# Performance work log

Measured on AMD Instinct MI355X. Metric: run time of the kernel, lower is better.

## Reference

```python
import jax, jax.numpy as jnp
import numpy as np

B, L, G, D = 32, 128, 64, 256
HD = 128; H = 2 * HD          # bidirectional LSTM hidden
N, K = 8, 4                   # nodes per graph, idx per node
NINP, NHID, NREL = 128, 32, 16
NTOK = 1000
E = B * N * N                 # all-pairs edges per graph, flattened
EPS = 1e-5


def setup_inputs() -> dict:
    key = jax.random.key(0)
    ks = jax.random.split(key, 40)
    rn = lambda i, shape, s: (s * jax.random.normal(ks[i], shape)).astype(jnp.float32)
    inp = {}
    inp["seq"] = jax.random.randint(ks[0], (B, L), 0, NTOK, dtype=jnp.int32)
    inp["pos2grp"] = jax.random.randint(ks[1], (B, L), 0, G, dtype=jnp.int32)
    inp["idx"] = jax.random.randint(ks[2], (B, N, K), 0, L, dtype=jnp.int32)
    ii = np.repeat(np.arange(N), N); jj = np.tile(np.arange(N), N)
    inp["u"] = jnp.asarray((np.arange(B)[:, None] * N + ii[None, :]).reshape(-1), dtype=jnp.int32)
    inp["v"] = jnp.asarray((np.arange(B)[:, None] * N + jj[None, :]).reshape(-1), dtype=jnp.int32)
    inp["mask"] = jax.random.uniform(ks[3], (E, NREL)) < 0.1
    inp["emb"] = rn(4, (NTOK, D), 1.0)
    # BiLSTM params (1 layer, 2 directions); gate order i,f,g,o
    inp["Wih_f"] = rn(5, (4 * HD, D), 0.05); inp["Whh_f"] = rn(6, (4 * HD, HD), 0.05)
    inp["bih_f"] = jnp.zeros((4 * HD,), jnp.float32); inp["bhh_f"] = jnp.zeros((4 * HD,), jnp.float32)
    inp["Wih_b"] = rn(7, (4 * HD, D), 0.05); inp["Whh_b"] = rn(8, (4 * HD, HD), 0.05)
    inp["bih_b"] = jnp.zeros((4 * HD,), jnp.float32); inp["bhh_b"] = jnp.zeros((4 * HD,), jnp.float32)
    inp["lin_src_w"] = rn(9, (NINP, H), 0.05); inp["lin_src_b"] = jnp.zeros((NINP,), jnp.float32)
    inp["lin_dst_w"] = rn(10, (NINP, H), 0.05); inp["lin_dst_b"] = jnp.zeros((NINP,), jnp.float32)
    inp["bn_src_g"] = jnp.ones((NINP,), jnp.float32); inp["bn_src_b"] = jnp.zeros((NINP,), jnp.float32)
    inp["bn_dst_g"] = jnp.ones((NINP,), jnp.float32); inp["bn_dst_b"] = jnp.zeros((NINP,), jnp.float32)
    inp["ntl_w"] = rn(11, (NREL, NHID, NINP, NINP), 0.001)
    inp["ntl_v"] = rn(12, (NREL, NHID, 2 * NINP), 0.001)
    inp["ntl_b"] = jnp.zeros((NREL, NHID, 1), jnp.float32)
    inp["ntl_u"] = rn(13, (NREL, 1, NHID), 0.001)
    inp["ntl_bn_g"] = jnp.ones((NREL * NHID,), jnp.float32)
    inp["ntl_bn_b"] = jnp.zeros((NREL * NHID,), jnp.float32)
    return inp


def _lstm(xs, Wih, Whh, bih, bhh):
    # xs: (T, B, D) -> (T, B, HD)
    nb = xs.shape[1]
    def step(carry, xt):
        h, c = carry
        g = xt @ Wih.T + h @ Whh.T + bih + bhh
        i, f, gg, o = jnp.split(g, 4, axis=-1)
        c = jax.nn.sigmoid(f) * c + jax.nn.sigmoid(i) * jnp.tanh(gg)
        h = jax.nn.sigmoid(o) * jnp.tanh(c)
        return (h, c), h
    init = (jnp.zeros((nb, HD), xs.dtype), jnp.zeros((nb, HD), xs.dtype))
    _, hs = jax.lax.scan(step, init, xs)
    return hs


def _bn(x, g, b):
    # training-mode BatchNorm1d over axis 0 (biased variance, as torch)
    m = x.mean(0)
    v = x.var(0)
    return (x - m) * jax.lax.rsqrt(v + EPS) * g + b


def _forward(emb, Wih_f, Whh_f, bih_f, bhh_f, Wih_b, Whh_b, bih_b, bhh_b,
             lin_src_w, lin_src_b, lin_dst_w, lin_dst_b,
             bn_src_g, bn_src_b, bn_dst_g, bn_dst_b,
             ntl_w, ntl_v, ntl_b, ntl_u, ntl_bn_g, ntl_bn_b,
             seq, pos2grp, idx, u, v):
    # 1) token embedding + scatter_sum into groups
    x_tok = emb[seq]                                         # (B,L,D)
    flat_ids = (pos2grp + jnp.arange(B, dtype=pos2grp.dtype)[:, None] * G).reshape(-1)
    x_grp = jax.ops.segment_sum(x_tok.reshape(B * L, D), flat_ids,
                                num_segments=B * G).reshape(B, G, D)
    # 2) BiLSTM over group sequence
    xs = x_grp.transpose(1, 0, 2)                            # (G,B,D)
    hf = _lstm(xs, Wih_f, Whh_f, bih_f, bhh_f)
    hb = _lstm(xs[::-1], Wih_b, Whh_b, bih_b, bhh_b)[::-1]
    h_grp = jnp.concatenate([hf, hb], -1).transpose(1, 0, 2) # (B,G,H)
    # 3) fancy-indexed gather h_grp[i, pos2grp[i, idx], :] + scatter_sum over K
    grp_of_idx = jnp.take_along_axis(pos2grp, idx.reshape(B, N * K), axis=1)
    h_sel = jnp.take_along_axis(h_grp, grp_of_idx[..., None], axis=1)  # (B,N*K,H)
    h = h_sel.reshape(B, N, K, H).sum(2).reshape(B * N, H)
    # 4) per-endpoint projection + batchnorm
    hd = _bn(h[u] @ lin_src_w.T + lin_src_b, bn_src_g, bn_src_b)  # (E,NINP)
    tl = _bn(h[v] @ lin_dst_w.T + lin_dst_b, bn_dst_g, bn_dst_b)
    # 5) neural tensor layer (bilinear=True)
    cat = jnp.concatenate([hd, tl], 1)                       # (E,2*NINP)
    linear = jnp.einsum('rhi,ei->rhe', ntl_v, cat)
    tmp = jnp.einsum('rhij,ei->rhej', ntl_w, hd)             # (NREL,NHID,E,NINP)
    bilinear = jnp.einsum('rhej,ej->rhe', tmp, tl)
    pre = bilinear + linear + ntl_b                          # (NREL,NHID,E)
    flat = pre.reshape(NREL * NHID, E).T                     # (E, NREL*NHID)
    act = jnp.tanh(_bn(flat, ntl_bn_g, ntl_bn_b).T.reshape(NREL, NHID, E))
    logit = jnp.einsum('rh,rhe->er', ntl_u[:, 0, :], act)    # (E,NREL)
    return logit


def reference(seq, pos2grp, idx, u, v, mask, emb,
              Wih_f, Whh_f, bih_f, bhh_f, Wih_b, Whh_b, bih_b, bhh_b,
              lin_src_w, lin_src_b, lin_dst_w, lin_dst_b,
              bn_src_g, bn_src_b, bn_dst_g, bn_dst_b,
              ntl_w, ntl_v, ntl_b, ntl_u, ntl_bn_g, ntl_bn_b):
    logit = _forward(emb, Wih_f, Whh_f, bih_f, bhh_f, Wih_b, Whh_b, bih_b, bhh_b,
                     lin_src_w, lin_src_b, lin_dst_w, lin_dst_b,
                     bn_src_g, bn_src_b, bn_dst_g, bn_dst_b,
                     ntl_w, ntl_v, ntl_b, ntl_u, ntl_bn_g, ntl_bn_b,
                     seq, pos2grp, idx, u, v)
    gt = logit > 0
    eq = gt == mask
    acc = eq.astype(jnp.float32).mean()
    gid = jnp.repeat(jnp.arange(B, dtype=jnp.int32), N * N)
    em = jax.ops.segment_min(jnp.all(eq, 1).astype(jnp.int32), gid, num_segments=B)
    emr = em.astype(jnp.float32).mean()
    nll_pos = -jnp.sum(jnp.where(mask, jax.nn.log_sigmoid(logit), 0.0)) / B
    nll_neg = -jnp.sum(jnp.where(mask, 0.0, jnp.log(1.0 + 1e-5 - jax.nn.sigmoid(logit)))) / B
    loss = nll_pos + nll_neg
    return logit, loss, acc, emr
```

## Files before the change

### kernel.cpp

```cpp
#include <hip/hip_runtime.h>
#include <math.h>

namespace {

constexpr int cB = 32, cL = 128, cG = 64, cD = 256;
constexpr int cHD = 128, cH = 256;
constexpr int cN = 8, cK = 4;
constexpr int cNI = 128, cRH = 512;
constexpr int cE = 2048;
constexpr float cEPS = 1e-5f;

typedef __bf16 bf16x8 __attribute__((ext_vector_type(8)));
typedef float f32x4 __attribute__((ext_vector_type(4)));

__device__ __forceinline__ f32x4 mfma16(bf16x8 a, bf16x8 b, f32x4 c) {
    return __builtin_amdgcn_mfma_f32_16x16x32_bf16(a, b, c, 0, 0, 0);
}

__device__ __forceinline__ float bf2f(unsigned short u) {
    unsigned int x = ((unsigned int)u) << 16;
    return __uint_as_float(x);
}
__device__ __forceinline__ unsigned short f2bf(float f) {
    unsigned int x = __float_as_uint(f);
    unsigned int r = (x + 0x7fffu + ((x >> 16) & 1u)) >> 16;
    return (unsigned short)r;
}
__device__ __forceinline__ float frcp(float x) { return __builtin_amdgcn_rcpf(x); }
__device__ __forceinline__ float fsig(float x) { return frcp(1.f + __expf(-x)); }
__device__ __forceinline__ float ftanh(float x) { return 1.f - 2.f * frcp(__expf(2.f * x) + 1.f); }
__device__ __forceinline__ float nls(float x) {
    return (x >= 0.f) ? log1pf(expf(-x)) : (log1pf(expf(x)) - x);
}
__device__ __forceinline__ bf16x8 cvt8(const float* __restrict__ p) {
    float4 a = *(const float4*)p, b = *(const float4*)(p + 4);
    bf16x8 v;
    v[0] = (__bf16)a.x; v[1] = (__bf16)a.y; v[2] = (__bf16)a.z; v[3] = (__bf16)a.w;
    v[4] = (__bf16)b.x; v[5] = (__bf16)b.y; v[6] = (__bf16)b.z; v[7] = (__bf16)b.w;
    return v;
}

__device__ __forceinline__ void bar_lgkm() {
    asm volatile("s_waitcnt lgkmcnt(0)\n\ts_barrier" ::: "memory");
}

__global__ void k_embed(const int* __restrict__ seq, const int* __restrict__ p2g,
                        const float* __restrict__ emb, float* __restrict__ x_seq) {
    __shared__ float xl[cG * cD];
    int b = blockIdx.x, t = threadIdx.x;
    for (int g = 0; g < cG; ++g) xl[g * cD + t] = 0.f;
    for (int l = 0; l < cL; ++l) {
        int tok = seq[b * cL + l];
        int g = p2g[b * cL + l];
        xl[g * cD + t] += emb[tok * cD + t];
    }
    for (int g = 0; g < cG; ++g)
        x_seq[(g * cB + b) * cD + t] = xl[g * cD + t];
}

__global__ __launch_bounds__(512) void k_gemm_in(
    const float* __restrict__ x_seq,
    const float* __restrict__ wih_f, const float* __restrict__ wih_b,
    const float* __restrict__ bih_f, const float* __restrict__ bhh_f,
    const float* __restrict__ bih_b, const float* __restrict__ bhh_b,
    float* __restrict__ pre) {
    int ns = blockIdx.x, g = blockIdx.y;
    int t = threadIdx.x;
    int w = t >> 6, l = t & 63, lc = l & 15, lk = l >> 4;
    int gn = ns * 128 + w * 16 + lc;
    const float* wrow = (gn < 512) ? (wih_f + (size_t)gn * cD)
                                   : (wih_b + (size_t)(gn - 512) * cD);
    const float* xb0 = x_seq + ((size_t)g * 32 + lc) * cD;
    const float* xb1 = x_seq + ((size_t)g * 32 + 16 + lc) * cD;
    f32x4 acc0 = {0.f, 0.f, 0.f, 0.f}, acc1 = {0.f, 0.f, 0.f, 0.f};
#pragma unroll
    for (int kf = 0; kf < 8; ++kf) {
        int ko = kf * 32 + lk * 8;
        bf16x8 a = cvt8(wrow + ko);
        bf16x8 b0 = cvt8(xb0 + ko);
        bf16x8 b1 = cvt8(xb1 + ko);
        acc0 = mfma16(a, b0, acc0);
        acc1 = mfma16(a, b1, acc1);
    }
    int nb = ns * 128 + w * 16 + lk * 4;
    float4 bv;
    if (nb < 512) {
        float4 u = *(const float4*)(bih_f + nb);
        float4 v = *(const float4*)(bhh_f + nb);
        bv = make_float4(u.x + v.x, u.y + v.y, u.z + v.z, u.w + v.w);
    } else {
        float4 u = *(const float4*)(bih_b + nb - 512);
        float4 v = *(const float4*)(bhh_b + nb - 512);
        bv = make_float4(u.x + v.x, u.y + v.y, u.z + v.z, u.w + v.w);
    }
    size_t base = ((size_t)g * 256 + (nb >> 2)) * 32;
    *(float4*)(pre + (base + lc) * 4) =
        make_float4(acc0[0] + bv.x, acc0[1] + bv.y, acc0[2] + bv.z, acc0[3] + bv.w);
    *(float4*)(pre + (base + 16 + lc) * 4) =
        make_float4(acc1[0] + bv.x, acc1[1] + bv.y, acc1[2] + bv.z, acc1[3] + bv.w);
}

__device__ __forceinline__ void lstm_step(
    f32x4 (&acc)[4], float (&cst)[4], const bf16x8 (&wf)[4][4],
    const unsigned short* __restrict__ hr, unsigned short* __restrict__ hw,
    const int (&rdo)[4], int wro,
    const float* __restrict__ preb, int gpre, bool dopre,
    unsigned short* __restrict__ hob, int g) {
    bf16x8 hf[4];
#pragma unroll
    for (int kf = 0; kf < 4; ++kf)
        hf[kf] = *(const bf16x8*)((const char*)hr + rdo[kf]);
#pragma unroll
    for (int kf = 0; kf < 4; ++kf)
#pragma unroll
        for (int q = 0; q < 4; ++q)
            acc[q] = mfma16(wf[q][kf], hf[kf], acc[q]);
    float hv[4];
#pragma unroll
    for (int r = 0; r < 4; ++r) {
        float ig = fsig(acc[0][r]);
        float fg = fsig(acc[1][r]);
        float gg = ftanh(acc[2][r]);
        float og = fsig(acc[3][r]);
        float cv = fg * cst[r] + ig * gg;
        cst[r] = cv;
        hv[r] = og * ftanh(cv);
    }
    if (dopre) {
#pragma unroll
        for (int q = 0; q < 4; ++q)
            acc[q] = *(const f32x4*)(preb + (size_t)gpre * 32768 + q * 4096);
    }
    unsigned int p0 = (unsigned int)f2bf(hv[0]) | ((unsigned int)f2bf(hv[1]) << 16);
    unsigned int p1 = (unsigned int)f2bf(hv[2]) | ((unsigned int)f2bf(hv[3]) << 16);
    *(uint2*)((char*)hw + wro) = make_uint2(p0, p1);
    *(uint2*)(hob + (size_t)g * 8192) = make_uint2(p0, p1);
    bar_lgkm();
}

__global__ __launch_bounds__(512, 2) void k_lstm_m(
    const float* __restrict__ pre,
    const float* __restrict__ whh_f, const float* __restrict__ whh_b,
    unsigned short* __restrict__ h_out) {
    __shared__ __align__(16) unsigned short hl[2][2048];
    int t = threadIdx.x;
    int w = t >> 6, l = t & 63, lc = l & 15, lk = l >> 4;
    int dir = blockIdx.x >> 1, bg = (blockIdx.x & 1) * 16;
    const float* whh = dir ? whh_b : whh_f;
    bf16x8 wf[4][4];
#pragma unroll
    for (int q = 0; q < 4; ++q) {
        int n = q * 128 + w * 16 + lc;
#pragma unroll
        for (int kf = 0; kf < 4; ++kf)
            wf[q][kf] = cvt8(whh + (size_t)n * 128 + kf * 32 + lk * 8);
    }
    *(uint2*)&hl[1][t * 4] = make_uint2(0u, 0u);
    const float* preb = pre + ((size_t)(dir * 128 + w * 4 + lk) * 32 + (bg + lc)) * 4;
    unsigned short* hob = h_out + ((size_t)(dir * 32 + bg + lc) * 128 + w * 16 + lk * 4);
    int rdo[4];
#pragma unroll
    for (int kf = 0; kf < 4; ++kf)
        rdo[kf] = (lc * 256 + kf * 64 + lk * 16) ^ (lc << 4);
    int wro = (lc * 256 + w * 32 + lk * 8) ^ (lc << 4);
    f32x4 accA[4], accB[4];
    float cst[4] = {0.f, 0.f, 0.f, 0.f};
    int g0 = dir ? 63 : 0;
    int sgn = dir ? -1 : 1;
#pragma unroll
    for (int q = 0; q < 4; ++q) accA[q] = *(const f32x4*)(preb + (size_t)g0 * 32768 + q * 4096);
#pragma unroll
    for (int q = 0; q < 4; ++q) accB[q] = *(const f32x4*)(preb + (size_t)(g0 + sgn) * 32768 + q * 4096);
    bar_lgkm();
    for (int s = 0; s < 64; s += 2) {
        int ga = g0 + sgn * s;
        lstm_step(accA, cst, wf, hl[1], hl[0], rdo, wro, preb, ga + 2 * sgn, s < 62, hob, ga);
        lstm_step(accB, cst, wf, hl[0], hl[1], rdo, wro, preb, ga + 3 * sgn, s < 61, hob, ga + sgn);
    }
}

__global__ __launch_bounds__(256) void k_gather(
    const int* __restrict__ idx, const int* __restrict__ p2g,
    const unsigned short* __restrict__ h_out, float* __restrict__ hsumT) {
    __shared__ float xr[32][257];
    int n0 = blockIdx.x * 32, t = threadIdx.x;
    int dirq = t >> 7, hh = t & 127;
    for (int nl = 0; nl < 32; ++nl) {
        int bn = n0 + nl;
        int b = bn >> 3;
        float acc = 0.f;
#pragma unroll
        for (int k = 0; k < cK; ++k) {
            int l = idx[bn * cK + k];
            int g = p2g[b * cL + l];
            acc += bf2f(h_out[(size_t)g * 8192 + (size_t)(dirq * 32 + b) * 128 + hh]);
        }
        xr[nl][t] = acc;
    }
    __syncthreads();
    int c_hi = t >> 5, nl = t & 31;
    for (int rep = 0; rep < 32; ++rep) {
        int c = rep * 8 + c_hi;
        hsumT[(size_t)c * 256 + n0 + nl] = xr[nl][c];
    }
}

__global__ __launch_bounds__(256) void k_proj_bn(
    const float* __restrict__ hsumT,
    const float* __restrict__ w_src, const float* __restrict__ b_src,
    const float* __restrict__ w_dst, const float* __restrict__ b_dst,
    const float* __restrict__ g_src, const float* __restrict__ bb_src,
    const float* __restrict__ g_dst, const float* __restrict__ bb_dst,
    float* __restrict__ hd_bn, float* __restrict__ tl_bn) {
    int which = blockIdx.x, c = blockIdx.y, t = threadIdx.x;
    __shared__ float ws[256];
    __shared__ float ssum[256], ssq[256];
    ws[t] = (which ? w_dst : w_src)[(size_t)c * cH + t];
    __syncthreads();
    float acc = (which ? b_dst : b_src)[c];
#pragma unroll 8
    for (int k = 0; k < cH; ++k)
        acc += ws[k] * hsumT[(size_t)k * 256 + t];
    ssum[t] = acc;
    ssq[t] = acc * acc;
    __syncthreads();
    for (int o = 128; o > 0; o >>= 1) {
        if (t < o) { ssum[t] += ssum[t + o]; ssq[t] += ssq[t + o]; }
        __syncthreads();
    }
    float mean = ssum[0] * (1.f / 256.f);
    float var = ssq[0] * (1.f / 256.f) - mean * mean;
    float gam = which ? g_dst[c] : g_src[c];
    float bet = which ? bb_dst[c] : bb_src[c];
    float scale = gam * rsqrtf(var + cEPS);
    (which ? tl_bn : hd_bn)[(size_t)t * cNI + c] = (acc - mean) * scale + bet;
}

__global__ __launch_bounds__(256, 2) void k_ntl_A(
    const float* __restrict__ hd_bn, const float* __restrict__ tl_bn,
    const float* __restrict__ ntl_w, const float* __restrict__ ntl_v,
    unsigned short* __restrict__ tmp,
    float* __restrict__ lsrc, float* __restrict__ ldst) {
    __shared__ __align__(16) unsigned short wl[128 * 128];
    __shared__ float vsh[256];
    int rh = blockIdx.x, t = threadIdx.x;
    int w = t >> 6, l = t & 63, lc = l & 15, lk = l >> 4;
    vsh[t] = ntl_v[(size_t)rh * 256 + t];
    {
        const float* wbase = ntl_w + (size_t)rh * 16384;
        int k = t >> 1, c0 = (t & 1) * 64;
        int sw = ((k >> 3) & 3) << 4;
#pragma unroll
        for (int u = 0; u < 8; ++u) {
            bf16x8 v = cvt8(wbase + k * 128 + c0 + u * 8);
            *(bf16x8*)((char*)wl + ((k * 256 + (c0 + u * 8) * 2) ^ sw)) = v;
        }
    }
    __syncthreads();
    {
        const float* hr = hd_bn + (size_t)t * cNI;
        const float* tr = tl_bn + (size_t)t * cNI;
        float a1 = 0.f, a2 = 0.f;
#pragma unroll 8
        for (int i = 0; i < cNI; i += 4) {
            float4 h4 = *(const float4*)(hr + i);
            float4 t4 = *(const float4*)(tr + i);
            a1 += h4.x * vsh[i] + h4.y * vsh[i + 1] + h4.z * vsh[i + 2] + h4.w * vsh[i + 3];
            a2 += t4.x * vsh[128 + i] + t4.y * vsh[128 + i + 1] + t4.z * vsh[128 + i + 2] + t4.w * vsh[128 + i + 3];
        }
        lsrc[(size_t)rh * 256 + t] = a1;
        ldst[(size_t)rh * 256 + t] = a2;
    }
    f32x4 acc[4][8] = {};
#pragma unroll
    for (int kf = 0; kf < 4; ++kf) {
        bf16x8 af[4];
#pragma unroll
        for (int mt = 0; mt < 4; ++mt) {
            int m = w * 64 + mt * 16 + lc;
            af[mt] = cvt8(hd_bn + (size_t)m * 128 + kf * 32 + lk * 8);
        }
#pragma unroll
        for (int nt = 0; nt < 8; ++nt) {
            int kb = (kf * 32 + lk * 8) * 256;
            int jb = (nt * 16 + lc) * 2;
            bf16x8 bv = *(const bf16x8*)((char*)wl + ((kb + jb) ^ (lk << 4)));
#pragma unroll
            for (int mt = 0; mt < 4; ++mt) acc[mt][nt] = mfma16(af[mt], bv, acc[mt][nt]);
        }
    }
#pragma unroll
    for (int mt = 0; mt < 4; ++mt) {
#pragma unroll
        for (int nt = 0; nt < 8; ++nt) {
            unsigned int lo = (unsigned int)f2bf(acc[mt][nt][0]) | ((unsigned int)f2bf(acc[mt][nt][1]) << 16);
            unsigned int hi = (unsigned int)f2bf(acc[mt][nt][2]) | ((unsigned int)f2bf(acc[mt][nt][3]) << 16);
            size_t off = (size_t)rh * 32768 + (size_t)((((w * 4 + mt) * 8 + nt) * 64 + l) * 4);
            *(uint2*)(tmp + off) = make_uint2(lo, hi);
        }
    }
}

__global__ __launch_bounds__(256) void k_ntl_B(
    const unsigned short* __restrict__ tmp, const float* __restrict__ tl_bn,
    const float* __restrict__ lsrc, const float* __restrict__ ldst,
    const float* __restrict__ ntl_b, float* __restrict__ pre2) {
    int bgid = blockIdx.x;
    int rh = blockIdx.y;
    int t = threadIdx.x;
    int n0 = bgid * 32;
    __shared__ float tm[32][132];
    __shared__ float tl[32][132];
    {
        const uint4* src = (const uint4*)(tmp + (size_t)rh * 32768 +
                                          (size_t)(bgid >> 1) * 8192 + (size_t)(bgid & 1) * 4096);
#pragma unroll
        for (int rep = 0; rep < 2; ++rep) {
            int q = t + rep * 256;
            uint4 uv = src[q];
            unsigned int wds[4] = {uv.x, uv.y, uv.z, uv.w};
            int e0 = q * 8;
#pragma unroll
            for (int ui = 0; ui < 4; ++ui) {
                int e = e0 + ui * 2;
                int mt_l = e >> 11;
                int nt = (e >> 8) & 7;
                int ln = (e >> 2) & 63;
                int r = e & 3;
                int m = mt_l * 16 + (ln >> 4) * 4 + r;
                int j = nt * 16 + (ln & 15);
                tm[m][j] = bf2f((unsigned short)(wds[ui] & 0xffff));
                tm[m + 1][j] = bf2f((unsigned short)(wds[ui] >> 16));
            }
        }
        int r = t >> 3;
        int c0 = (t & 7) * 16;
        const float4* fsrc = (const float4*)(tl_bn + (size_t)(n0 + r) * cNI + c0);
        float4 f0 = fsrc[0], f1 = fsrc[1], f2v = fsrc[2], f3 = fsrc[3];
        float* frow = &tl[r][c0];
        frow[0] = f0.x; frow[1] = f0.y; frow[2] = f0.z; frow[3] = f0.w;
        frow[4] = f1.x; frow[5] = f1.y; frow[6] = f1.z; frow[7] = f1.w;
        frow[8] = f2v.x; frow[9] = f2v.y; frow[10] = f2v.z; frow[11] = f2v.w;
        frow[12] = f3.x; frow[13] = f3.y; frow[14] = f3.z; frow[15] = f3.w;
    }
    __syncthreads();
    int b_l = t >> 6, p = t & 63, i = p >> 3, j = p & 7;
    const float* ta = &tm[b_l * 8 + i][0];
    const float* tb = &tl[b_l * 8 + j][0];
    float s = 0.f;
#pragma unroll 8
    for (int k = 0; k < 128; ++k) s += ta[k] * tb[k];
    int e = bgid * 256 + t;
    int bglob = bgid * 4 + b_l;
    int un = bglob * 8 + i, vn = bglob * 8 + j;
    pre2[(size_t)rh * cE + e] = s + lsrc[(size_t)rh * 256 + un] + ldst[(size_t)rh * 256 + vn] + ntl_b[rh];
}

__global__ void k_bn2(const float* __restrict__ pre2,
                      const float* __restrict__ g, const float* __restrict__ bta,
                      float* __restrict__ scale, float* __restrict__ shift) {
    int rh = blockIdx.x, t = threadIdx.x;
    const float* row = pre2 + (size_t)rh * cE;
    float s = 0.f, q = 0.f;
#pragma unroll
    for (int ii = 0; ii < 8; ++ii) {
        float v = row[ii * 256 + t];
        s += v; q += v * v;
    }
    __shared__ float ssum[256], ssq[256];
    ssum[t] = s; ssq[t] = q;
    __syncthreads();
    for (int o = 128; o > 0; o >>= 1) {
        if (t < o) { ssum[t] += ssum[t + o]; ssq[t] += ssq[t + o]; }
        __syncthreads();
    }
    if (t == 0) {
        float mean = ssum[0] * (1.f / 2048.f);
        float var = ssq[0] * (1.f / 2048.f) - mean * mean;
        float sc = g[rh] * rsqrtf(var + cEPS);
        scale[rh] = sc;
        shift[rh] = bta[rh] - mean * sc;
    }
}

__global__ __launch_bounds__(256) void k_final(
    const float* __restrict__ pre2,
    const float* __restrict__ scale, const float* __restrict__ shift,
    const float* __restrict__ ntl_u, const int* __restrict__ mask,
    float* __restrict__ out, float* __restrict__ part) {
    int r = blockIdx.y, et = blockIdx.x;
    int t = threadIdx.x;
    int e = et * 256 + t;
    float a = 0.f;
#pragma unroll
    for (int h = 0; h < 32; ++h) {
        int rh = r * 32 + h;
        float p = pre2[(size_t)rh * cE + e];
        a += ntl_u[rh] * ftanh(fmaf(p, scale[rh], shift[rh]));
    }
    out[(size_t)e * 16 + r] = a;
    int m = mask[(size_t)e * 16 + r];
    bool mb = (m != 0);
    bool eq = ((a > 0.f) == mb);
    float nll = mb ? nls(a) : -logf(1.f / (1.f + expf(a)) + 1e-5f);
    float corr = eq ? 1.f : 0.f;
    unsigned long long bal = __ballot(eq);
    float em = (bal == ~0ull) ? 1.f : 0.f;
#pragma unroll
    for (int o = 32; o > 0; o >>= 1) {
        nll += __shfl_down(nll, o);
        corr += __shfl_down(corr, o);
    }
    if ((t & 63) == 0) {
        int bg = et * 4 + (t >> 6);
        float* p = part + ((size_t)bg * 16 + r) * 4;
        p[0] = nll; p[1] = corr; p[2] = em;
    }
}

__global__ void k_loss_fin(const float* __restrict__ part, float* __restrict__ out) {
    int t = threadIdx.x;
    float nll = 0.f, corr = 0.f, em = 0.f;
    if (t < 32) {
        em = 1.f;
        for (int r = 0; r < 16; ++r) {
            const float* p = part + ((size_t)t * 16 + r) * 4;
            nll += p[0]; corr += p[1]; em = fminf(em, p[2]);
        }
    }
#pragma unroll
    for (int o = 32; o > 0; o >>= 1) {
        nll += __shfl_down(nll, o);
        corr += __shfl_down(corr, o);
        em += __shfl_down(em, o);
    }
    if (t == 0) {
        out[32768] = nll / 32.f;
        out[32769] = corr / 32768.f;
        out[32770] = em / 32.f;
    }
}

}

extern "C" void kernel_launch(void* const* d_in, const int* in_sizes, int n_in,
                              void* d_out, int out_size, void* d_ws, size_t ws_size,
                              hipStream_t stream) {
    (void)in_sizes; (void)n_in; (void)out_size; (void)ws_size;
    const int* seq = (const int*)d_in[0];
    const int* p2g = (const int*)d_in[1];
    const int* idx = (const int*)d_in[2];
    const int* mask = (const int*)d_in[5];
    const float* emb = (const float*)d_in[6];
    const float* wih_f = (const float*)d_in[7];
    const float* whh_f = (const float*)d_in[8];
    const float* bih_f = (const float*)d_in[9];
    const float* bhh_f = (const float*)d_in[10];
    const float* wih_b = (const float*)d_in[11];
    const float* whh_b = (const float*)d_in[12];
    const float* bih_b = (const float*)d_in[13];
    const float* bhh_b = (const float*)d_in[14];
    const float* lsw = (const float*)d_in[15];
    const float* lsb = (const float*)d_in[16];
    const float* ldw = (const float*)d_in[17];
    const float* ldb = (const float*)d_in[18];
    const float* bn_sg = (const float*)d_in[19];
    const float* bn_sb = (const float*)d_in[20];
    const float* bn_dg = (const float*)d_in[21];
    const float* bn_db = (const float*)d_in[22];
    const float* ntlw = (const float*)d_in[23];
    const float* ntlv = (const float*)d_in[24];
    const float* ntlb = (const float*)d_in[25];
    const float* ntlu = (const float*)d_in[26];
    const float* bn2g = (const float*)d_in[27];
    const float* bn2b = (const float*)d_in[28];
    float* out = (float*)d_out;
    char* ws = (char*)d_ws;

    float* x_seq = (float*)(ws + 0);
    float* pre = (float*)(ws + 2097152);
    unsigned short* tmp = (unsigned short*)(ws + 0);
    size_t off = 33554432;
    unsigned short* h_out = (unsigned short*)(ws + off); off += 1048576;
    float* hsumT = (float*)(ws + off); off += 262144;
    float* hd_bn = (float*)(ws + off); off += 131072;
    float* tl_bn = (float*)(ws + off); off += 131072;
    float* lsrc = (float*)(ws + off); off += 524288;
    float* ldst = (float*)(ws + off); off += 524288;
    float* pre2 = (float*)(ws + off); off += 4194304;
    float* scale = (float*)(ws + off); off += 2048;
    float* shift = (float*)(ws + off); off += 2048;
    float* part = (float*)(ws + off); off += 8192;

    k_embed<<<32, 256, 0, stream>>>(seq, p2g, emb, x_seq);
    k_gemm_in<<<dim3(8, 64), 512, 0, stream>>>(x_seq, wih_f, wih_b, bih_f, bhh_f, bih_b, bhh_b, pre);
    k_lstm_m<<<4, 512, 0, stream>>>(pre, whh_f, whh_b, h_out);
    k_gather<<<8, 256, 0, stream>>>(idx, p2g, h_out, hsumT);
    k_proj_bn<<<dim3(2, 128), 256, 0, stream>>>(hsumT, lsw, lsb, ldw, ldb,
                                                bn_sg, bn_sb, bn_dg, bn_db, hd_bn, tl_bn);
    k_ntl_A<<<512, 256, 0, stream>>>(hd_bn, tl_bn, ntlw, ntlv, tmp, lsrc, ldst);
    k_ntl_B<<<dim3(8, 512), 256, 0, stream>>>(tmp, tl_bn, lsrc, ldst, ntlb, pre2);
    k_bn2<<<512, 256, 0, stream>>>(pre2, bn2g, bn2b, scale, shift);
    k_final<<<dim3(8, 16), 256, 0, stream>>>(pre2, scale, shift, ntlu, mask, out, part);
    k_loss_fin<<<1, 64, 0, stream>>>(part, out);
}
```

Baseline: 190.7 us.

## Fuse BN2 stats into ntl_B, parallelize gather, batch embed loads

Removes the separate k_bn2 kernel. k_ntl_B now uses 64-thread blocks that each compute a 2x2 register tile of outputs and write per-block partial sum and sum-of-squares. k_final reduces those partials into BN scale and shift in shared memory. k_gather now launches one block per node instead of 8 blocks that loop over 32 nodes, and k_embed stages token and group indices in shared memory and issues four embedding loads per iteration. These changes aim to cut one launch plus a full read of pre2 and to raise parallelism in the small kernels, at the cost of uncoalesced transposed stores in gather and fewer threads per block in ntl_B.

New measurement: 178.1 us. 6.6% less time.

```diff
diff --git a/kernel.cpp b/kernel.cpp
--- a/kernel.cpp
+++ b/kernel.cpp
@@ -44,15 +44,25 @@
     asm volatile("s_waitcnt lgkmcnt(0)\n\ts_barrier" ::: "memory");
 }
 
-__global__ void k_embed(const int* __restrict__ seq, const int* __restrict__ p2g,
-                        const float* __restrict__ emb, float* __restrict__ x_seq) {
+__global__ __launch_bounds__(256) void k_embed(
+    const int* __restrict__ seq, const int* __restrict__ p2g,
+    const float* __restrict__ emb, float* __restrict__ x_seq) {
     __shared__ float xl[cG * cD];
+    __shared__ int toks[cL], grps[cL];
     int b = blockIdx.x, t = threadIdx.x;
+    if (t < 128) toks[t] = seq[b * cL + t];
+    else grps[t - 128] = p2g[b * cL + (t - 128)];
     for (int g = 0; g < cG; ++g) xl[g * cD + t] = 0.f;
-    for (int l = 0; l < cL; ++l) {
-        int tok = seq[b * cL + l];
-        int g = p2g[b * cL + l];
-        xl[g * cD + t] += emb[tok * cD + t];
+    __syncthreads();
+    for (int l = 0; l < cL; l += 4) {
+        float v0 = emb[(size_t)toks[l + 0] * cD + t];
+        float v1 = emb[(size_t)toks[l + 1] * cD + t];
+        float v2 = emb[(size_t)toks[l + 2] * cD + t];
+        float v3 = emb[(size_t)toks[l + 3] * cD + t];
+        xl[grps[l + 0] * cD + t] += v0;
+        xl[grps[l + 1] * cD + t] += v1;
+        xl[grps[l + 2] * cD + t] += v2;
+        xl[grps[l + 3] * cD + t] += v3;
     }
     for (int g = 0; g < cG; ++g)
         x_seq[(g * cB + b) * cD + t] = xl[g * cD + t];
@@ -182,27 +192,18 @@
 __global__ __launch_bounds__(256) void k_gather(
     const int* __restrict__ idx, const int* __restrict__ p2g,
     const unsigned short* __restrict__ h_out, float* __restrict__ hsumT) {
-    __shared__ float xr[32][257];
-    int n0 = blockIdx.x * 32, t = threadIdx.x;
+    int bn = blockIdx.x;
+    int b = bn >> 3;
+    int t = threadIdx.x;
     int dirq = t >> 7, hh = t & 127;
-    for (int nl = 0; nl < 32; ++nl) {
-        int bn = n0 + nl;
-        int b = bn >> 3;
-        float acc = 0.f;
-#pragma unroll
-        for (int k = 0; k < cK; ++k) {
-            int l = idx[bn * cK + k];
-            int g = p2g[b * cL + l];
-            acc += bf2f(h_out[(size_t)g * 8192 + (size_t)(dirq * 32 + b) * 128 + hh]);
-        }
-        xr[nl][t] = acc;
-    }
-    __syncthreads();
-    int c_hi = t >> 5, nl = t & 31;
-    for (int rep = 0; rep < 32; ++rep) {
-        int c = rep * 8 + c_hi;
-        hsumT[(size_t)c * 256 + n0 + nl] = xr[nl][c];
-    }
+    int l0 = idx[bn * cK + 0], l1 = idx[bn * cK + 1];
+    int l2 = idx[bn * cK + 2], l3 = idx[bn * cK + 3];
+    int g0 = p2g[b * cL + l0], g1 = p2g[b * cL + l1];
+    int g2 = p2g[b * cL + l2], g3 = p2g[b * cL + l3];
+    size_t ro = (size_t)(dirq * 32 + b) * 128 + hh;
+    float a = bf2f(h_out[(size_t)g0 * 8192 + ro]) + bf2f(h_out[(size_t)g1 * 8192 + ro]) +
+              bf2f(h_out[(size_t)g2 * 8192 + ro]) + bf2f(h_out[(size_t)g3 * 8192 + ro]);
+    hsumT[(size_t)t * 256 + bn] = a;
 }
 
 __global__ __launch_bounds__(256) void k_proj_bn(
@@ -301,10 +302,11 @@
     }
 }
 
-__global__ __launch_bounds__(256) void k_ntl_B(
+__global__ __launch_bounds__(64) void k_ntl_B(
     const unsigned short* __restrict__ tmp, const float* __restrict__ tl_bn,
     const float* __restrict__ lsrc, const float* __restrict__ ldst,
-    const float* __restrict__ ntl_b, float* __restrict__ pre2) {
+    const float* __restrict__ ntl_b, float* __restrict__ pre2,
+    float2* __restrict__ part2) {
     int bgid = blockIdx.x;
     int rh = blockIdx.y;
     int t = threadIdx.x;
@@ -315,8 +317,8 @@
         const uint4* src = (const uint4*)(tmp + (size_t)rh * 32768 +
                                           (size_t)(bgid >> 1) * 8192 + (size_t)(bgid & 1) * 4096);
 #pragma unroll
-        for (int rep = 0; rep < 2; ++rep) {
-            int q = t + rep * 256;
+        for (int rep = 0; rep < 8; ++rep) {
+            int q = t + rep * 64;
             uint4 uv = src[q];
             unsigned int wds[4] = {uv.x, uv.y, uv.z, uv.w};
             int e0 = q * 8;
@@ -333,70 +335,88 @@
                 tm[m + 1][j] = bf2f((unsigned short)(wds[ui] >> 16));
             }
         }
-        int r = t >> 3;
-        int c0 = (t & 7) * 16;
-        const float4* fsrc = (const float4*)(tl_bn + (size_t)(n0 + r) * cNI + c0);
-        float4 f0 = fsrc[0], f1 = fsrc[1], f2v = fsrc[2], f3 = fsrc[3];
-        float* frow = &tl[r][c0];
-        frow[0] = f0.x; frow[1] = f0.y; frow[2] = f0.z; frow[3] = f0.w;
-        frow[4] = f1.x; frow[5] = f1.y; frow[6] = f1.z; frow[7] = f1.w;
-        frow[8] = f2v.x; frow[9] = f2v.y; frow[10] = f2v.z; frow[11] = f2v.w;
-        frow[12] = f3.x; frow[13] = f3.y; frow[14] = f3.z; frow[15] = f3.w;
+#pragma unroll
+        for (int rep = 0; rep < 4; ++rep) {
+            int tt = t + rep * 64;
+            int r = tt >> 3;
+            int c0 = (tt & 7) * 16;
+            const float4* fsrc = (const float4*)(tl_bn + (size_t)(n0 + r) * cNI + c0);
+            float4 f0 = fsrc[0], f1 = fsrc[1], f2v = fsrc[2], f3 = fsrc[3];
+            float* frow = &tl[r][c0];
+            frow[0] = f0.x; frow[1] = f0.y; frow[2] = f0.z; frow[3] = f0.w;
+            frow[4] = f1.x; frow[5] = f1.y; frow[6] = f1.z; frow[7] = f1.w;
+            frow[8] = f2v.x; frow[9] = f2v.y; frow[10] = f2v.z; frow[11] = f2v.w;
+            frow[12] = f3.x; frow[13] = f3.y; frow[14] = f3.z; frow[15] = f3.w;
+        }
     }
     __syncthreads();
-    int b_l = t >> 6, p = t & 63, i = p >> 3, j = p & 7;
-    const float* ta = &tm[b_l * 8 + i][0];
-    const float* tb = &tl[b_l * 8 + j][0];
-    float s = 0.f;
-#pragma unroll 8
-    for (int k = 0; k < 128; ++k) s += ta[k] * tb[k];
-    int e = bgid * 256 + t;
+    int b_l = t >> 4, i2 = (t >> 2) & 3, j2 = t & 3;
+    const float* ta0 = &tm[b_l * 8 + i2][0];
+    const float* ta1 = &tm[b_l * 8 + i2 + 4][0];
+    const float* tb0 = &tl[b_l * 8 + j2][0];
+    const float* tb1 = &tl[b_l * 8 + j2 + 4][0];
+    float s00 = 0.f, s01 = 0.f, s10 = 0.f, s11 = 0.f;
+#pragma unroll 4
+    for (int k = 0; k < 128; ++k) {
+        float a0 = ta0[k], a1 = ta1[k], b0 = tb0[k], b1 = tb1[k];
+        s00 += a0 * b0; s01 += a0 * b1; s10 += a1 * b0; s11 += a1 * b1;
+    }
     int bglob = bgid * 4 + b_l;
-    int un = bglob * 8 + i, vn = bglob * 8 + j;
-    pre2[(size_t)rh * cE + e] = s + lsrc[(size_t)rh * 256 + un] + ldst[(size_t)rh * 256 + vn] + ntl_b[rh];
-}
-
-__global__ void k_bn2(const float* __restrict__ pre2,
-                      const float* __restrict__ g, const float* __restrict__ bta,
-                      float* __restrict__ scale, float* __restrict__ shift) {
-    int rh = blockIdx.x, t = threadIdx.x;
-    const float* row = pre2 + (size_t)rh * cE;
-    float s = 0.f, q = 0.f;
-#pragma unroll
-    for (int ii = 0; ii < 8; ++ii) {
-        float v = row[ii * 256 + t];
-        s += v; q += v * v;
-    }
-    __shared__ float ssum[256], ssq[256];
-    ssum[t] = s; ssq[t] = q;
-    __syncthreads();
-    for (int o = 128; o > 0; o >>= 1) {
-        if (t < o) { ssum[t] += ssum[t + o]; ssq[t] += ssq[t + o]; }
-        __syncthreads();
-    }
-    if (t == 0) {
-        float mean = ssum[0] * (1.f / 2048.f);
-        float var = ssq[0] * (1.f / 2048.f) - mean * mean;
-        float sc = g[rh] * rsqrtf(var + cEPS);
-        scale[rh] = sc;
-        shift[rh] = bta[rh] - mean * sc;
-    }
+    float nb = ntl_b[rh];
+    const float* ls = lsrc + (size_t)rh * 256 + bglob * 8;
+    const float* ld = ldst + (size_t)rh * 256 + bglob * 8;
+    float* pr = pre2 + (size_t)rh * cE + bgid * 256 + b_l * 64;
+    float vs[4];
+    vs[0] = s00 + ls[i2] + ld[j2] + nb;
+    vs[1] = s01 + ls[i2] + ld[j2 + 4] + nb;
+    vs[2] = s10 + ls[i2 + 4] + ld[j2] + nb;
+    vs[3] = s11 + ls[i2 + 4] + ld[j2 + 4] + nb;
+    pr[i2 * 8 + j2] = vs[0];
+    pr[i2 * 8 + j2 + 4] = vs[1];
+    pr[(i2 + 4) * 8 + j2] = vs[2];
+    pr[(i2 + 4) * 8 + j2 + 4] = vs[3];
+    float sm = vs[0] + vs[1] + vs[2] + vs[3];
+    float sq = vs[0] * vs[0] + vs[1] * vs[1] + vs[2] * vs[2] + vs[3] * vs[3];
+#pragma unroll
+    for (int o = 32; o > 0; o >>= 1) {
+        sm += __shfl_down(sm, o);
+        sq += __shfl_down(sq, o);
+    }
+    if (t == 0) part2[(size_t)rh * 8 + bgid] = make_float2(sm, sq);
 }
 
 __global__ __launch_bounds__(256) void k_final(
-    const float* __restrict__ pre2,
-    const float* __restrict__ scale, const float* __restrict__ shift,
+    const float* __restrict__ pre2, const float2* __restrict__ part2,
+    const float* __restrict__ g2, const float* __restrict__ b2,
     const float* __restrict__ ntl_u, const int* __restrict__ mask,
     float* __restrict__ out, float* __restrict__ part) {
     int r = blockIdx.y, et = blockIdx.x;
     int t = threadIdx.x;
+    __shared__ float sc[32], sh[32];
+    {
+        int rh_l = t >> 3, slot = t & 7;
+        int rh = r * 32 + rh_l;
+        float2 pp = part2[(size_t)rh * 8 + slot];
+        float S = pp.x, Q = pp.y;
+        S += __shfl_xor(S, 1); Q += __shfl_xor(Q, 1);
+        S += __shfl_xor(S, 2); Q += __shfl_xor(Q, 2);
+        S += __shfl_xor(S, 4); Q += __shfl_xor(Q, 4);
+        if (slot == 0) {
+            float mean = S * (1.f / 2048.f);
+            float var = Q * (1.f / 2048.f) - mean * mean;
+            float scv = g2[rh] * rsqrtf(var + cEPS);
+            sc[rh_l] = scv;
+            sh[rh_l] = b2[rh] - mean * scv;
+        }
+    }
+    __syncthreads();
     int e = et * 256 + t;
     float a = 0.f;
 #pragma unroll
     for (int h = 0; h < 32; ++h) {
         int rh = r * 32 + h;
         float p = pre2[(size_t)rh * cE + e];
-        a += ntl_u[rh] * ftanh(fmaf(p, scale[rh], shift[rh]));
+        a += ntl_u[rh] * ftanh(fmaf(p, sc[h], sh[h]));
     }
     out[(size_t)e * 16 + r] = a;
     int m = mask[(size_t)e * 16 + r];
@@ -488,19 +508,17 @@
     float* lsrc = (float*)(ws + off); off += 524288;
     float* ldst = (float*)(ws + off); off += 524288;
     float* pre2 = (float*)(ws + off); off += 4194304;
-    float* scale = (float*)(ws + off); off += 2048;
-    float* shift = (float*)(ws + off); off += 2048;
+    float2* part2 = (float2*)(ws + off); off += 32768;
     float* part = (float*)(ws + off); off += 8192;
 
     k_embed<<<32, 256, 0, stream>>>(seq, p2g, emb, x_seq);
     k_gemm_in<<<dim3(8, 64), 512, 0, stream>>>(x_seq, wih_f, wih_b, bih_f, bhh_f, bih_b, bhh_b, pre);
     k_lstm_m<<<4, 512, 0, stream>>>(pre, whh_f, whh_b, h_out);
-    k_gather<<<8, 256, 0, stream>>>(idx, p2g, h_out, hsumT);
+    k_gather<<<256, 256, 0, stream>>>(idx, p2g, h_out, hsumT);
     k_proj_bn<<<dim3(2, 128), 256, 0, stream>>>(hsumT, lsw, lsb, ldw, ldb,
                                                 bn_sg, bn_sb, bn_dg, bn_db, hd_bn, tl_bn);
     k_ntl_A<<<512, 256, 0, stream>>>(hd_bn, tl_bn, ntlw, ntlv, tmp, lsrc, ldst);
-    k_ntl_B<<<dim3(8, 512), 256, 0, stream>>>(tmp, tl_bn, lsrc, ldst, ntlb, pre2);
-    k_bn2<<<512, 256, 0, stream>>>(pre2, bn2g, bn2b, scale, shift);
-    k_final<<<dim3(8, 16), 256, 0, stream>>>(pre2, scale, shift, ntlu, mask, out, part);
+    k_ntl_B<<<dim3(8, 512), 64, 0, stream>>>(tmp, tl_bn, lsrc, ldst, ntlb, pre2, part2);
+    k_final<<<dim3(8, 16), 256, 0, stream>>>(pre2, part2, bn2g, bn2b, ntlu, mask, out, part);
     k_loss_fin<<<1, 64, 0, stream>>>(part, out);
 }
```
